# Kernel optimization log

Hardware: AMD Instinct MI355X
Metric: run time of the kernel (lower is better)

## Reference

```python
import jax, jax.numpy as jnp
import numpy as np

TEMPERATURE = 0.07
EPS = 1e-12  # matches F.normalize eps

def _l2norm(x, axis):
    n = jnp.sqrt(jnp.sum(x * x, axis=axis, keepdims=True))
    return x / jnp.maximum(n, EPS)

def setup_inputs() -> dict:
    key = jax.random.key(0)
    features = jax.random.normal(key, (512, 256), dtype=jnp.float32)
    return {"features": features}

def reference(features) -> jnp.ndarray:
    B = features.shape[0]
    f = _l2norm(features, axis=1)                      # [B, D]
    fi = f[:, None, :]                                 # broadcast over j
    fj = f[None, :, :]                                 # broadcast over i
    mutual = fi * fj                                   # [B, B, D]
    gate_i = fi * mutual
    gate_j = fj * mutual
    # torch broadcasting: + features adds f[j, k] along trailing dims
    feats_self_i = _l2norm(fi * gate_i + f, axis=2)
    feats_other_i = _l2norm(fi * gate_j + f, axis=2)
    feats_other_j = _l2norm(fj * gate_i + f, axis=2)
    # note: features_self_j is computed in the original but never used in any dot product

    raw_self_i = jnp.einsum('ik,ijk->ij', f, feats_self_i) / TEMPERATURE
    raw_self_j = jnp.einsum('ik,ijk->ij', f, feats_other_j) / TEMPERATURE  # (original uses other_j here)
    raw_other_i = jnp.einsum('ik,ijk->ij', f, feats_other_i) / TEMPERATURE
    raw_other_j = jnp.einsum('ik,ijk->ij', f, feats_other_j) / TEMPERATURE

    logits_mask = 1.0 - jnp.eye(B, dtype=f.dtype)      # zero out diagonal
    exp_sum = (jnp.exp(raw_self_i) + jnp.exp(raw_self_j)
               + jnp.exp(raw_other_i) + jnp.exp(raw_other_j)) * logits_mask
    vs_all = jnp.sum(exp_sum, axis=1, keepdims=True)   # [B, 1]

    log_prob = raw_self_i - jnp.log(vs_all)            # [B, B]
    mean_log_prob_pos = jnp.sum(log_prob, axis=1) / B
    loss = -jnp.mean(mean_log_prob_pos)
    return loss
```

## Files before the change

### kernel.cpp

```cpp
#include <hip/hip_runtime.h>
#include <math.h>

#define Bq 512
#define Dq 256

__device__ __forceinline__ float waveReduceSum(float v) {
    #pragma unroll
    for (int off = 32; off > 0; off >>= 1)
        v += __shfl_xor(v, off, 64);
    return v;
}

__global__ __launch_bounds__(256) void prep_kernel(
        const float* __restrict__ feat,
        float* __restrict__ fT, float* __restrict__ norms,
        int* __restrict__ counter) {
    int i = blockIdx.x;
    int k = threadIdx.x;
    float x = feat[i * Dq + k];
    float ss = waveReduceSum(x * x);
    __shared__ float wsum[4];
    int wid = threadIdx.x >> 6, lane = threadIdx.x & 63;
    if (lane == 0) wsum[wid] = ss;
    __syncthreads();
    float tot = wsum[0] + wsum[1] + wsum[2] + wsum[3];
    float n = fmaxf(sqrtf(tot), 1e-12f);
    fT[k * Bq + i] = x / n;
    if (k == 0) norms[i] = n;
    if (i == 0 && k == 0) *counter = 0;
}

__global__ __launch_bounds__(512) void pair_kernel(
        const float* __restrict__ feat,
        const float* __restrict__ fT, const float* __restrict__ norms,
        float* __restrict__ tws, int* __restrict__ counter,
        float* __restrict__ out) {
    const int i = blockIdx.x;
    const int t = threadIdx.x;

    __shared__ __align__(16) float s_c1[Dq];
    __shared__ __align__(16) float s_c2[Dq];
    __shared__ __align__(16) float s_a1[Dq];
    __shared__ __align__(16) float s_a2[Dq];
    if (t < Dq) {
        float a  = feat[i * Dq + t] / norms[i];
        float a2 = a * a;
        float c0 = 1.0f + a2 * a;
        s_a1[t] = a;
        s_a2[t] = a2;
        s_c1[t] = a * c0;
        s_c2[t] = c0 * c0;
    }
    __syncthreads();

    float du = 0.f, nu = 0.f, dv = 0.f, nv = 0.f;
    const float* __restrict__ bp = fT + t;

    #pragma unroll 2
    for (int k0 = 0; k0 < Dq; k0 += 8) {
        float b[8];
        #pragma unroll
        for (int u = 0; u < 8; ++u) b[u] = bp[(k0 + u) * Bq];

        float4 q1a = *(const float4*)(s_c1 + k0), q1b = *(const float4*)(s_c1 + k0 + 4);
        float4 q2a = *(const float4*)(s_c2 + k0), q2b = *(const float4*)(s_c2 + k0 + 4);
        float4 q3a = *(const float4*)(s_a1 + k0), q3b = *(const float4*)(s_a1 + k0 + 4);
        float4 q4a = *(const float4*)(s_a2 + k0), q4b = *(const float4*)(s_a2 + k0 + 4);
        const float c1[8] = {q1a.x, q1a.y, q1a.z, q1a.w, q1b.x, q1b.y, q1b.z, q1b.w};
        const float c2[8] = {q2a.x, q2a.y, q2a.z, q2a.w, q2b.x, q2b.y, q2b.z, q2b.w};
        const float a1[8] = {q3a.x, q3a.y, q3a.z, q3a.w, q3b.x, q3b.y, q3b.z, q3b.w};
        const float a2[8] = {q4a.x, q4a.y, q4a.z, q4a.w, q4b.x, q4b.y, q4b.z, q4b.w};

        #pragma unroll
        for (int u = 0; u < 8; ++u) {
            float b1 = b[u];
            float bb = b1 * b1;
            float w  = fmaf(a2[u], b1, 1.0f);
            float wb = w * b1;
            du = fmaf(c1[u], b1, du);
            nu = fmaf(c2[u], bb, nu);
            dv = fmaf(a1[u], wb, dv);
            nv = fmaf(wb,    wb, nv);
        }
    }

    const float Tinv = 1.0f / 0.07f;
    float raw_s = du / fmaxf(sqrtf(nu), 1e-12f) * Tinv;
    float raw_o = dv / fmaxf(sqrtf(nv), 1e-12f) * Tinv;

    float sS = raw_s;
    float sV = (t == i) ? 0.f : (expf(raw_s) + 3.0f * expf(raw_o));

    sS = waveReduceSum(sS);
    sV = waveReduceSum(sV);
    __shared__ float redS[8], redV[8];
    int wid = t >> 6, lane = t & 63;
    if (lane == 0) { redS[wid] = sS; redV[wid] = sV; }
    __syncthreads();

    __shared__ int s_last;
    if (t == 0) {
        float S = 0.f, V = 0.f;
        #pragma unroll
        for (int w2 = 0; w2 < 8; ++w2) { S += redS[w2]; V += redV[w2]; }
        float ti = S * (1.0f / Bq) - logf(V);
        __hip_atomic_store(&tws[i], ti, __ATOMIC_RELEASE, __HIP_MEMORY_SCOPE_AGENT);
        int old = __hip_atomic_fetch_add(counter, 1, __ATOMIC_ACQ_REL,
                                         __HIP_MEMORY_SCOPE_AGENT);
        s_last = (old == Bq - 1) ? 1 : 0;
    }
    __syncthreads();

    if (s_last) {
        float v = __hip_atomic_load(&tws[t], __ATOMIC_RELAXED,
                                    __HIP_MEMORY_SCOPE_AGENT);
        float r = waveReduceSum(v);
        __shared__ float red[8];
        if (lane == 0) red[wid] = r;
        __syncthreads();
        if (t == 0) {
            float s = 0.f;
            #pragma unroll
            for (int w = 0; w < 8; ++w) s += red[w];
            out[0] = -s / (float)Bq;
        }
    }
}

extern "C" void kernel_launch(void* const* d_in, const int* in_sizes, int n_in,
                              void* d_out, int out_size, void* d_ws, size_t ws_size,
                              hipStream_t stream) {
    const float* feat = (const float*)d_in[0];
    float* ws = (float*)d_ws;
    float* fT    = ws;
    float* norms = fT + Bq * Dq;
    float* tws   = norms + Bq;
    int*   counter = (int*)(tws + Bq);

    prep_kernel<<<Bq, Dq, 0, stream>>>(feat, fT, norms, counter);
    pair_kernel<<<Bq, 512, 0, stream>>>(feat, fT, norms, tws, counter,
                                        (float*)d_out);
}
```

Measured before the change: 86.37 us.

## Compute two columns per thread with packed float2 math and split final reduction

```diff
diff --git a/kernel.cpp b/kernel.cpp
--- a/kernel.cpp
+++ b/kernel.cpp
@@ -3,6 +3,8 @@
 
 #define Bq 512
 #define Dq 256
+
+typedef float v2f __attribute__((ext_vector_type(2)));
 
 __device__ __forceinline__ float waveReduceSum(float v) {
     #pragma unroll
@@ -13,8 +15,7 @@
 
 __global__ __launch_bounds__(256) void prep_kernel(
         const float* __restrict__ feat,
-        float* __restrict__ fT, float* __restrict__ norms,
-        int* __restrict__ counter) {
+        float* __restrict__ fT, float* __restrict__ norms) {
     int i = blockIdx.x;
     int k = threadIdx.x;
     float x = feat[i * Dq + k];
@@ -27,22 +28,21 @@
     float n = fmaxf(sqrtf(tot), 1e-12f);
     fT[k * Bq + i] = x / n;
     if (k == 0) norms[i] = n;
-    if (i == 0 && k == 0) *counter = 0;
 }
 
-__global__ __launch_bounds__(512) void pair_kernel(
+__global__ __launch_bounds__(256) void pair_kernel(
         const float* __restrict__ feat,
         const float* __restrict__ fT, const float* __restrict__ norms,
-        float* __restrict__ tws, int* __restrict__ counter,
-        float* __restrict__ out) {
+        float* __restrict__ Sv, float* __restrict__ Vv) {
     const int i = blockIdx.x;
     const int t = threadIdx.x;
+    const int j0 = 2 * t;
 
     __shared__ __align__(16) float s_c1[Dq];
     __shared__ __align__(16) float s_c2[Dq];
     __shared__ __align__(16) float s_a1[Dq];
     __shared__ __align__(16) float s_a2[Dq];
-    if (t < Dq) {
+    {
         float a  = feat[i * Dq + t] / norms[i];
         float a2 = a * a;
         float c0 = 1.0f + a2 * a;
@@ -53,77 +53,83 @@
     }
     __syncthreads();
 
-    float du = 0.f, nu = 0.f, dv = 0.f, nv = 0.f;
-    const float* __restrict__ bp = fT + t;
+    v2f du = {0.f, 0.f}, nu = {0.f, 0.f}, dv = {0.f, 0.f}, nv = {0.f, 0.f};
+    const float* __restrict__ bp = fT + j0;
+    const v2f one2 = {1.0f, 1.0f};
 
-    #pragma unroll 2
     for (int k0 = 0; k0 < Dq; k0 += 8) {
-        float b[8];
+        v2f b[8];
         #pragma unroll
-        for (int u = 0; u < 8; ++u) b[u] = bp[(k0 + u) * Bq];
+        for (int u = 0; u < 8; ++u)
+            b[u] = *(const v2f*)(bp + (k0 + u) * Bq);
 
         float4 q1a = *(const float4*)(s_c1 + k0), q1b = *(const float4*)(s_c1 + k0 + 4);
         float4 q2a = *(const float4*)(s_c2 + k0), q2b = *(const float4*)(s_c2 + k0 + 4);
         float4 q3a = *(const float4*)(s_a1 + k0), q3b = *(const float4*)(s_a1 + k0 + 4);
         float4 q4a = *(const float4*)(s_a2 + k0), q4b = *(const float4*)(s_a2 + k0 + 4);
-        const float c1[8] = {q1a.x, q1a.y, q1a.z, q1a.w, q1b.x, q1b.y, q1b.z, q1b.w};
-        const float c2[8] = {q2a.x, q2a.y, q2a.z, q2a.w, q2b.x, q2b.y, q2b.z, q2b.w};
-        const float a1[8] = {q3a.x, q3a.y, q3a.z, q3a.w, q3b.x, q3b.y, q3b.z, q3b.w};
-        const float a2[8] = {q4a.x, q4a.y, q4a.z, q4a.w, q4b.x, q4b.y, q4b.z, q4b.w};
+        const float c1a[8] = {q1a.x, q1a.y, q1a.z, q1a.w, q1b.x, q1b.y, q1b.z, q1b.w};
+        const float c2a[8] = {q2a.x, q2a.y, q2a.z, q2a.w, q2b.x, q2b.y, q2b.z, q2b.w};
+        const float a1a[8] = {q3a.x, q3a.y, q3a.z, q3a.w, q3b.x, q3b.y, q3b.z, q3b.w};
+        const float a2a[8] = {q4a.x, q4a.y, q4a.z, q4a.w, q4b.x, q4b.y, q4b.z, q4b.w};
 
         #pragma unroll
         for (int u = 0; u < 8; ++u) {
-            float b1 = b[u];
-            float bb = b1 * b1;
-            float w  = fmaf(a2[u], b1, 1.0f);
-            float wb = w * b1;
-            du = fmaf(c1[u], b1, du);
-            nu = fmaf(c2[u], bb, nu);
-            dv = fmaf(a1[u], wb, dv);
-            nv = fmaf(wb,    wb, nv);
+            v2f bv = b[u];
+            v2f bb = bv * bv;
+            v2f a2s = {a2a[u], a2a[u]};
+            v2f w   = __builtin_elementwise_fma(a2s, bv, one2);
+            v2f wb  = w * bv;
+            v2f c1s = {c1a[u], c1a[u]};
+            v2f c2s = {c2a[u], c2a[u]};
+            v2f a1s = {a1a[u], a1a[u]};
+            du = __builtin_elementwise_fma(c1s, bv, du);
+            nu = __builtin_elementwise_fma(c2s, bb, nu);
+            dv = __builtin_elementwise_fma(a1s, wb, dv);
+            nv = __builtin_elementwise_fma(wb,  wb, nv);
         }
     }
 
     const float Tinv = 1.0f / 0.07f;
-    float raw_s = du / fmaxf(sqrtf(nu), 1e-12f) * Tinv;
-    float raw_o = dv / fmaxf(sqrtf(nv), 1e-12f) * Tinv;
+    float raw_s0 = du.x / fmaxf(sqrtf(nu.x), 1e-12f) * Tinv;
+    float raw_o0 = dv.x / fmaxf(sqrtf(nv.x), 1e-12f) * Tinv;
+    float raw_s1 = du.y / fmaxf(sqrtf(nu.y), 1e-12f) * Tinv;
+    float raw_o1 = dv.y / fmaxf(sqrtf(nv.y), 1e-12f) * Tinv;
 
-    float sS = raw_s;
-    float sV = (t == i) ? 0.f : (expf(raw_s) + 3.0f * expf(raw_o));
+    float sS = raw_s0 + raw_s1;
+    float sV = 0.f;
+    if (j0 != i)     sV += expf(raw_s0) + 3.0f * expf(raw_o0);
+    if (j0 + 1 != i) sV += expf(raw_s1) + 3.0f * expf(raw_o1);
 
     sS = waveReduceSum(sS);
     sV = waveReduceSum(sV);
-    __shared__ float redS[8], redV[8];
+    __shared__ float redS[4], redV[4];
     int wid = t >> 6, lane = t & 63;
     if (lane == 0) { redS[wid] = sS; redV[wid] = sV; }
     __syncthreads();
-
-    __shared__ int s_last;
     if (t == 0) {
         float S = 0.f, V = 0.f;
         #pragma unroll
-        for (int w2 = 0; w2 < 8; ++w2) { S += redS[w2]; V += redV[w2]; }
-        float ti = S * (1.0f / Bq) - logf(V);
-        __hip_atomic_store(&tws[i], ti, __ATOMIC_RELEASE, __HIP_MEMORY_SCOPE_AGENT);
-        int old = __hip_atomic_fetch_add(counter, 1, __ATOMIC_ACQ_REL,
-                                         __HIP_MEMORY_SCOPE_AGENT);
-        s_last = (old == Bq - 1) ? 1 : 0;
+        for (int w2 = 0; w2 < 4; ++w2) { S += redS[w2]; V += redV[w2]; }
+        Sv[i] = S;
+        Vv[i] = V;
     }
+}
+
+__global__ __launch_bounds__(512) void final_kernel(
+        const float* __restrict__ Sv, const float* __restrict__ Vv,
+        float* __restrict__ out) {
+    int i = threadIdx.x;
+    float t = Sv[i] * (1.0f / Bq) - logf(Vv[i]);
+    t = waveReduceSum(t);
+    __shared__ float red[8];
+    int wid = i >> 6, lane = i & 63;
+    if (lane == 0) red[wid] = t;
     __syncthreads();
-
-    if (s_last) {
-        float v = __hip_atomic_load(&tws[t], __ATOMIC_RELAXED,
-                                    __HIP_MEMORY_SCOPE_AGENT);
-        float r = waveReduceSum(v);
-        __shared__ float red[8];
-        if (lane == 0) red[wid] = r;
-        __syncthreads();
-        if (t == 0) {
-            float s = 0.f;
-            #pragma unroll
-            for (int w = 0; w < 8; ++w) s += red[w];
-            out[0] = -s / (float)Bq;
-        }
+    if (i == 0) {
+        float s = 0.f;
+        #pragma unroll
+        for (int w = 0; w < 8; ++w) s += red[w];
+        out[0] = -s / (float)Bq;
     }
 }
 
@@ -134,10 +140,10 @@
     float* ws = (float*)d_ws;
     float* fT    = ws;
     float* norms = fT + Bq * Dq;
-    float* tws   = norms + Bq;
-    int*   counter = (int*)(tws + Bq);
+    float* Sv    = norms + Bq;
+    float* Vv    = Sv + Bq;
 
-    prep_kernel<<<Bq, Dq, 0, stream>>>(feat, fT, norms, counter);
-    pair_kernel<<<Bq, 512, 0, stream>>>(feat, fT, norms, tws, counter,
-                                        (float*)d_out);
+    prep_kernel<<<Bq, Dq, 0, stream>>>(feat, fT, norms);
+    pair_kernel<<<Bq, 256, 0, stream>>>(feat, fT, norms, Sv, Vv);
+    final_kernel<<<1, Bq, 0, stream>>>(Sv, Vv, (float*)d_out);
 }
```

New measurement: 74.30 us. 1.16x faster.
